# Optimization experiments

Hardware: AMD Instinct MI355X
Metric: run time of the kernel (lower is better)

Reference implementation:

```python
import jax, jax.numpy as jnp
import numpy as np

N, K, F, H, C = 16384, 16, 3, 64, 10


def setup_inputs() -> dict:
    key = jax.random.key(0)
    ks = jax.random.split(key, 6)
    pos = jax.random.normal(ks[0], (N, F), jnp.float32)
    batch = jnp.zeros((N,), jnp.int32)  # single graph
    W1 = jax.random.normal(ks[1], (2 * F, H), jnp.float32) * 0.1
    b1 = jnp.zeros((H,), jnp.float32)
    W2 = jax.random.normal(ks[2], (2 * H, H), jnp.float32) * 0.1
    b2 = jnp.zeros((H,), jnp.float32)
    Wc = jax.random.normal(ks[3], (H, C), jnp.float32) * 0.1
    bc = jnp.zeros((C,), jnp.float32)
    return {"pos": pos, "batch": batch, "W1": W1, "b1": b1,
            "W2": W2, "b2": b2, "Wc": Wc, "bc": bc}


def knn_graph(pos, k):
    # brute-force knn with self-loops (loop=True): self has distance 0
    sq = jnp.sum(pos * pos, axis=1)
    d = sq[:, None] + sq[None, :] - 2.0 * (pos @ pos.T)  # [N, N]
    _, idx = jax.lax.top_k(-d, k)  # [N, k] nearest neighbor indices (incl. self)
    return idx


def edge_conv(x, idx, W, b):
    # message for edge j->i: Linear(concat(x_i, x_j - x_i)); aggregate by max over neighbors
    n, k = idx.shape
    xi = x[:, None, :]               # [N, 1, F]
    xj = x[idx]                      # [N, k, F]
    msg = jnp.concatenate([jnp.broadcast_to(xi, (n, k, x.shape[1])), xj - xi], axis=-1)
    m = msg @ W + b                  # [N, k, H]
    return jnp.max(m, axis=1)        # [N, H]


def reference(pos, batch, W1, b1, W2, b2, Wc, bc):
    idx = knn_graph(pos, K)
    h = jax.nn.relu(edge_conv(pos, idx, W1, b1))
    h = jax.nn.relu(edge_conv(h, idx, W2, b2))
    g = jax.ops.segment_max(h, batch, num_segments=1)  # global max pool -> [1, H]
    return g @ Wc + bc
```

## Files before the change

### kernel.cpp

```cpp
#include <hip/hip_runtime.h>

#define NPTS 16384
#define KNN 16
#define HID 64
#define NCLS 10

#define WPB 4
#define QPB 8
#define SCAP 128
#define GRPQ 32
#define NITER 16
#define TPAD 576

typedef float v2f __attribute__((ext_vector_type(2)));

__device__ __forceinline__ v2f pdist(v2f Qx, v2f Qy, v2f Qz, v2f X, v2f Y, v2f Z, v2f W) {
    return __builtin_elementwise_fma(Qx, X,
            __builtin_elementwise_fma(Qy, Y,
             __builtin_elementwise_fma(Qz, Z, W)));
}

__device__ __forceinline__ float distm2(float qx, float qy, float qz, float4 c) {
    return fmaf(qx, c.x, fmaf(qy, c.y, fmaf(qz, c.z, c.w)));
}

__device__ __forceinline__ float __frfl(float x) {
    return __int_as_float(__builtin_amdgcn_readfirstlane(__float_as_int(x)));
}

__device__ __forceinline__ unsigned long long dkey(float v, int j) {
    unsigned u = __float_as_uint(v);
    u = (u & 0x80000000u) ? ~u : (u | 0x80000000u);
    return ((unsigned long long)u << 32) | (unsigned)j;
}

__device__ __forceinline__ unsigned long long shfl_xor_u64(unsigned long long x, int m) {
    unsigned hi = (unsigned)__shfl_xor((int)(x >> 32), m, 64);
    unsigned lo = (unsigned)__shfl_xor((int)(x & 0xffffffffu), m, 64);
    return ((unsigned long long)hi << 32) | lo;
}

__device__ __forceinline__ void wave_top16_16(unsigned long long (&key)[16], int lane,
                                              int q, int* __restrict__ idx) {
    int outj = 0x7fffffff;
    for (int r = 0; r < 16; ++r) {
        unsigned long long gm = key[0];
#pragma unroll
        for (int s = 1; s < 16; ++s) gm = key[s] < gm ? key[s] : gm;
#pragma unroll
        for (int st = 1; st < 64; st <<= 1) {
            unsigned long long o = shfl_xor_u64(gm, st);
            gm = o < gm ? o : gm;
        }
        if (lane == r) outj = (int)(gm & 0xffffffffu);
#pragma unroll
        for (int s = 0; s < 16; ++s)
            if (key[s] == gm) key[s] = ~0ull;
    }
    if (lane < 16) idx[q * KNN + lane] = outj;
}

__global__ void prep_kernel(const float* __restrict__ pos, float4* __restrict__ pos4,
                            float4* __restrict__ pm2, float4* __restrict__ pm2t) {
    int i = blockIdx.x * 256 + threadIdx.x;
    if (i < NPTS) {
        float x = pos[3 * i], y = pos[3 * i + 1], z = pos[3 * i + 2];
        float sq = fmaf(x, x, fmaf(y, y, z * z));
        pos4[i] = make_float4(x, y, z, sq);
        pm2[i] = make_float4(-2.f * x, -2.f * y, -2.f * z, sq);
    }
    if (i < NPTS / 2) {
        int p = i;
        float x0 = pos[6 * p],     y0 = pos[6 * p + 1], z0 = pos[6 * p + 2];
        float x1 = pos[6 * p + 3], y1 = pos[6 * p + 4], z1 = pos[6 * p + 5];
        float w0 = fmaf(x0, x0, fmaf(y0, y0, z0 * z0));
        float w1 = fmaf(x1, x1, fmaf(y1, y1, z1 * z1));
        int g = p >> 6, l = p & 63;
        pm2t[g * 128 + l]      = make_float4(-2.f * x0, -2.f * x1, -2.f * y0, -2.f * y1);
        pm2t[g * 128 + 64 + l] = make_float4(-2.f * z0, -2.f * z1, w0, w1);
    }
}

__global__ __launch_bounds__(256) void knn_kernel(const float4* __restrict__ pos4,
                                                  const float4* __restrict__ pm2,
                                                  const float4* __restrict__ pm2t,
                                                  int* __restrict__ idx) {
    __shared__ unsigned long long keys[QPB][SCAP];
    __shared__ int knt[QPB];
    __shared__ float smin[QPB][WPB][16];
    int tid = threadIdx.x;
    int lane = tid & 63;
    int w = tid >> 6;
    int qb = blockIdx.x * QPB;
    v2f Qx[QPB], Qy[QPB], Qz[QPB];
#pragma unroll
    for (int i = 0; i < QPB; ++i) {
        float4 t4 = pos4[qb + i];
        float ax = __frfl(t4.x), ay = __frfl(t4.y), az = __frfl(t4.z);
        Qx[i] = (v2f){ax, ax}; Qy[i] = (v2f){ay, ay}; Qz[i] = (v2f){az, az};
    }
    const float4* pt = pm2t + (size_t)w * (GRPQ * 128) + lane;

    float mn[QPB];
#pragma unroll
    for (int i = 0; i < QPB; ++i) mn[i] = INFINITY;
    {
        float4 aXY0 = pt[0],   aZW0 = pt[64],  aXY1 = pt[128], aZW1 = pt[192];
        float4 bXY0 = pt[256], bZW0 = pt[320], bXY1 = pt[384], bZW1 = pt[448];
        int off = 512;
#pragma unroll 2
        for (int t = 0; t < NITER; ++t) {
            v2f X0 = {aXY0.x, aXY0.y}, Y0 = {aXY0.z, aXY0.w};
            v2f Z0 = {aZW0.x, aZW0.y}, W0 = {aZW0.z, aZW0.w};
            v2f X1 = {aXY1.x, aXY1.y}, Y1 = {aXY1.z, aXY1.w};
            v2f Z1 = {aZW1.x, aZW1.y}, W1 = {aZW1.z, aZW1.w};
#pragma unroll
            for (int i = 0; i < QPB; ++i) {
                v2f D0 = pdist(Qx[i], Qy[i], Qz[i], X0, Y0, Z0, W0);
                v2f D1 = pdist(Qx[i], Qy[i], Qz[i], X1, Y1, Z1, W1);
                mn[i] = fminf(mn[i], fminf(D0.x, D0.y));
                mn[i] = fminf(mn[i], fminf(D1.x, D1.y));
            }
            aXY0 = bXY0; aZW0 = bZW0; aXY1 = bXY1; aZW1 = bZW1;
            bXY0 = pt[off]; bZW0 = pt[off + 64]; bXY1 = pt[off + 128]; bZW1 = pt[off + 192];
            off += 256;
        }
    }
#pragma unroll
    for (int i = 0; i < QPB; ++i) {
        float m = mn[i];
        m = fminf(m, __shfl_xor(m, 16, 64));
        m = fminf(m, __shfl_xor(m, 32, 64));
        if (lane < 16) smin[i][w][lane] = m;
    }
    if (tid < QPB) knt[tid] = 0;
    __syncthreads();

    float tq[QPB];
#pragma unroll
    for (int i = 0; i < QPB; ++i) {
        int s = lane & 15;
        float m = fminf(fminf(smin[i][0][s], smin[i][1][s]),
                        fminf(smin[i][2][s], smin[i][3][s]));
        m = fmaxf(m, __shfl_xor(m, 1, 64));
        m = fmaxf(m, __shfl_xor(m, 2, 64));
        m = fmaxf(m, __shfl_xor(m, 4, 64));
        m = fmaxf(m, __shfl_xor(m, 8, 64));
        tq[i] = __frfl(m);
    }

    {
        float4 aXY0 = pt[0],   aZW0 = pt[64],  aXY1 = pt[128], aZW1 = pt[192];
        float4 bXY0 = pt[256], bZW0 = pt[320], bXY1 = pt[384], bZW1 = pt[448];
        int off = 512;
        int pbase = w * (GRPQ * 64);
#pragma unroll 2
        for (int t = 0; t < NITER; ++t) {
            v2f X0 = {aXY0.x, aXY0.y}, Y0 = {aXY0.z, aXY0.w};
            v2f Z0 = {aZW0.x, aZW0.y}, W0 = {aZW0.z, aZW0.w};
            v2f X1 = {aXY1.x, aXY1.y}, Y1 = {aXY1.z, aXY1.w};
            v2f Z1 = {aZW1.x, aZW1.y}, W1 = {aZW1.z, aZW1.w};
            int j00 = 2 * (pbase + t * 128 + lane);
            int j10 = j00 + 128;
#pragma unroll
            for (int i = 0; i < QPB; ++i) {
                v2f D0 = pdist(Qx[i], Qy[i], Qz[i], X0, Y0, Z0, W0);
                v2f D1 = pdist(Qx[i], Qy[i], Qz[i], X1, Y1, Z1, W1);
                float m01 = fminf(fminf(D0.x, D0.y), fminf(D1.x, D1.y));
                if (__any(m01 <= tq[i])) {
                    if (D0.x <= tq[i]) { int s = atomicAdd(&knt[i], 1); if (s < SCAP) keys[i][s] = dkey(D0.x, j00); }
                    if (D0.y <= tq[i]) { int s = atomicAdd(&knt[i], 1); if (s < SCAP) keys[i][s] = dkey(D0.y, j00 + 1); }
                    if (D1.x <= tq[i]) { int s = atomicAdd(&knt[i], 1); if (s < SCAP) keys[i][s] = dkey(D1.x, j10); }
                    if (D1.y <= tq[i]) { int s = atomicAdd(&knt[i], 1); if (s < SCAP) keys[i][s] = dkey(D1.y, j10 + 1); }
                }
            }
            aXY0 = bXY0; aZW0 = bZW0; aXY1 = bXY1; aZW1 = bZW1;
            bXY0 = pt[off]; bZW0 = pt[off + 64]; bXY1 = pt[off + 128]; bZW1 = pt[off + 448 - 256];
            bXY1 = pt[off + 128]; bZW1 = pt[off + 192];
            off += 256;
        }
    }
    __syncthreads();

#pragma unroll
    for (int e = 0; e < 2; ++e) {
        int qi = w * 2 + e;
        int q = qb + qi;
        int ntot = knt[qi];
        if (ntot <= SCAP) {
            unsigned long long k0 = (lane < ntot) ? keys[qi][lane] : ~0ull;
            unsigned long long k1 = (lane + 64 < ntot) ? keys[qi][lane + 64] : ~0ull;
            int r0 = 0, r1 = 0;
            int t = 0;
            for (; t + 8 <= ntot; t += 8) {
                unsigned long long a0 = keys[qi][t + 0], a1 = keys[qi][t + 1];
                unsigned long long a2 = keys[qi][t + 2], a3 = keys[qi][t + 3];
                unsigned long long a4 = keys[qi][t + 4], a5 = keys[qi][t + 5];
                unsigned long long a6 = keys[qi][t + 6], a7 = keys[qi][t + 7];
                r0 += (int)(a0 < k0) + (int)(a1 < k0) + (int)(a2 < k0) + (int)(a3 < k0)
                    + (int)(a4 < k0) + (int)(a5 < k0) + (int)(a6 < k0) + (int)(a7 < k0);
                r1 += (int)(a0 < k1) + (int)(a1 < k1) + (int)(a2 < k1) + (int)(a3 < k1)
                    + (int)(a4 < k1) + (int)(a5 < k1) + (int)(a6 < k1) + (int)(a7 < k1);
            }
            for (; t < ntot; ++t) {
                unsigned long long k = keys[qi][t];
                r0 += (int)(k < k0);
                r1 += (int)(k < k1);
            }
            if (lane < ntot && r0 < KNN) idx[q * KNN + r0] = (int)(k0 & 0xffffffffu);
            if (lane + 64 < ntot && r1 < KNN) idx[q * KNN + r1] = (int)(k1 & 0xffffffffu);
        } else {
            float tqq = tq[qi];
            float ax = Qx[qi].x, ay = Qy[qi].x, az = Qz[qi].x;
            unsigned long long key[16];
#pragma unroll
            for (int u = 0; u < 16; ++u) key[u] = ~0ull;
            for (int j = lane; j < NPTS; j += 64) {
                float v = distm2(ax, ay, az, pm2[j]);
                unsigned long long k = dkey(v, j);
                if (v <= tqq && k < key[15]) {
#pragma unroll
                    for (int s = 0; s < 16; ++s) {
                        unsigned long long a = k < key[s] ? k : key[s];
                        unsigned long long b = k < key[s] ? key[s] : k;
                        key[s] = a;
                        k = b;
                    }
                }
            }
            wave_top16_16(key, lane, q, idx);
        }
    }
}

__global__ __launch_bounds__(256) void ec12_kernel(const float4* __restrict__ pos4,
                                                   const int* __restrict__ idx,
                                                   const float* __restrict__ W1,
                                                   const float* __restrict__ b1,
                                                   const float* __restrict__ W2,
                                                   const float* __restrict__ b2,
                                                   float* __restrict__ C2,
                                                   float* __restrict__ Y2) {
    __shared__ float h1s[16][64];
    int t = threadIdx.x & 63;
    int w = threadIdx.x >> 6;
    int pb = blockIdx.x * 16 + w * 4;
    float w0 = W1[0 * HID + t], w1 = W1[1 * HID + t], w2 = W1[2 * HID + t];
    float v0 = W1[3 * HID + t], v1 = W1[4 * HID + t], v2 = W1[5 * HID + t];
    float bt1 = b1[t];
#pragma unroll
    for (int i = 0; i < 4; ++i) {
        int p = pb + i;
        float4 xi = pos4[p];
        float C = bt1 + xi.x * (w0 - v0) + xi.y * (w1 - v1) + xi.z * (w2 - v2);
        const int4* ip = (const int4*)(idx + (size_t)p * KNN);
        int4 n0 = ip[0], n1 = ip[1], n2 = ip[2], n3 = ip[3];
        int jj[16] = {n0.x, n0.y, n0.z, n0.w, n1.x, n1.y, n1.z, n1.w,
                      n2.x, n2.y, n2.z, n2.w, n3.x, n3.y, n3.z, n3.w};
        float m = -INFINITY;
#pragma unroll
        for (int k = 0; k < KNN; ++k) {
            float4 xj = pos4[jj[k]];
            m = fmaxf(m, fmaf(xj.x, v0, fmaf(xj.y, v1, xj.z * v2)));
        }
        h1s[w * 4 + i][t] = fmaxf(C + m, 0.f);
    }
    __syncthreads();
    float aa[4] = {0.f, 0.f, 0.f, 0.f};
    float ab[4] = {0.f, 0.f, 0.f, 0.f};
#pragma unroll 8
    for (int f = 0; f < 64; ++f) {
        float wa = W2[f * HID + t];
        float wb = W2[(64 + f) * HID + t];
#pragma unroll
        for (int i = 0; i < 4; ++i) {
            float h = h1s[w * 4 + i][f];
            aa[i] = fmaf(h, wa, aa[i]);
            ab[i] = fmaf(h, wb, ab[i]);
        }
    }
    float bt = b2[t];
#pragma unroll
    for (int i = 0; i < 4; ++i) {
        C2[(pb + i) * HID + t] = bt + aa[i] - ab[i];
        Y2[(pb + i) * HID + t] = ab[i];
    }
}

__global__ __launch_bounds__(256) void ec2_maxpool_kernel(const float* __restrict__ C2,
                                                          const float* __restrict__ Y2,
                                                          const int* __restrict__ idx,
                                                          float* __restrict__ gpartial) {
    int t = threadIdx.x & 63;
    int lp = threadIdx.x >> 6;
    int p = blockIdx.x * 4 + lp;
    const int4* ip = (const int4*)(idx + (size_t)p * KNN);
    int4 n0 = ip[0], n1 = ip[1], n2 = ip[2], n3 = ip[3];
    int jj[16] = {n0.x, n0.y, n0.z, n0.w, n1.x, n1.y, n1.z, n1.w,
                  n2.x, n2.y, n2.z, n2.w, n3.x, n3.y, n3.z, n3.w};
    float m = -INFINITY;
#pragma unroll
    for (int k = 0; k < KNN; ++k) {
        m = fmaxf(m, Y2[jj[k] * HID + t]);
    }
    float val = fmaxf(C2[p * HID + t] + m, 0.f);
    __shared__ float red[4][64];
    red[lp][t] = val;
    __syncthreads();
    if (lp == 0) {
        float g = fmaxf(fmaxf(red[0][t], red[1][t]), fmaxf(red[2][t], red[3][t]));
        gpartial[blockIdx.x * 64 + t] = g;
    }
}

__global__ __launch_bounds__(256) void greduce2_kernel(const float* __restrict__ gpartial,
                                                       float* __restrict__ gp2) {
    __shared__ float red[4][64];
    int f = threadIdx.x & 63;
    int w = threadIdx.x >> 6;
    int r0 = blockIdx.x * 16 + w * 4;
    float m = -INFINITY;
#pragma unroll
    for (int r = 0; r < 4; ++r) m = fmaxf(m, gpartial[(r0 + r) * 64 + f]);
    red[w][f] = m;
    __syncthreads();
    if (w == 0)
        gp2[blockIdx.x * 64 + f] =
            fmaxf(fmaxf(red[0][f], red[1][f]), fmaxf(red[2][f], red[3][f]));
}

__global__ __launch_bounds__(256) void tail2_kernel(const float* __restrict__ gp2,
                                                    const float* __restrict__ Wc,
                                                    const float* __restrict__ bc,
                                                    float* __restrict__ out) {
    __shared__ float red[4][64];
    __shared__ float g[64];
    int f = threadIdx.x & 63;
    int w = threadIdx.x >> 6;
    float m = -INFINITY;
    for (int i = w; i < 256; i += 4) m = fmaxf(m, gp2[i * 64 + f]);
    red[w][f] = m;
    __syncthreads();
    if (w == 0) g[f] = fmaxf(fmaxf(red[0][f], red[1][f]), fmaxf(red[2][f], red[3][f]));
    __syncthreads();
    if (threadIdx.x < NCLS) {
        float a = bc[threadIdx.x];
#pragma unroll
        for (int h = 0; h < HID; ++h) a = fmaf(g[h], Wc[h * NCLS + threadIdx.x], a);
        out[threadIdx.x] = a;
    }
}

extern "C" void kernel_launch(void* const* d_in, const int* in_sizes, int n_in,
                              void* d_out, int out_size, void* d_ws, size_t ws_size,
                              hipStream_t stream) {
    const float* pos = (const float*)d_in[0];
    const float* W1 = (const float*)d_in[2];
    const float* b1 = (const float*)d_in[3];
    const float* W2 = (const float*)d_in[4];
    const float* b2 = (const float*)d_in[5];
    const float* Wc = (const float*)d_in[6];
    const float* bc = (const float*)d_in[7];
    float* out = (float*)d_out;

    char* ws = (char*)d_ws;
    size_t o = 0;
    auto alloc = [&](size_t bytes) { size_t r = o; o += (bytes + 255) & ~size_t(255); return r; };
    size_t fm = (size_t)NPTS * HID * 4;
    size_t o_pos4 = alloc((size_t)NPTS * 16);
    size_t o_pm2 = alloc((size_t)NPTS * 16);
    size_t o_pm2t = alloc((size_t)(NPTS + TPAD) * 16);
    size_t o_idx = alloc((size_t)NPTS * KNN * 4);
    size_t o_C2 = alloc(fm);
    size_t o_Y2 = alloc(fm);
    size_t o_gp = alloc((size_t)(NPTS / 4) * HID * 4);
    size_t o_gp2 = alloc((size_t)256 * HID * 4);

    float4* pos4 = (float4*)(ws + o_pos4);
    float4* pm2 = (float4*)(ws + o_pm2);
    float4* pm2t = (float4*)(ws + o_pm2t);
    int* idx = (int*)(ws + o_idx);
    float* C2 = (float*)(ws + o_C2);
    float* Y2 = (float*)(ws + o_Y2);
    float* gp = (float*)(ws + o_gp);
    float* gp2 = (float*)(ws + o_gp2);

    hipMemsetAsync(pm2t + NPTS, 0, TPAD * sizeof(float4), stream);

    prep_kernel<<<NPTS / 256, 256, 0, stream>>>(pos, pos4, pm2, pm2t);
    knn_kernel<<<NPTS / QPB, 256, 0, stream>>>(pos4, pm2, pm2t, idx);
    ec12_kernel<<<NPTS / 16, 256, 0, stream>>>(pos4, idx, W1, b1, W2, b2, C2, Y2);
    ec2_maxpool_kernel<<<NPTS / 4, 256, 0, stream>>>(C2, Y2, idx, gp);
    greduce2_kernel<<<256, 256, 0, stream>>>(gp, gp2);
    tail2_kernel<<<1, 256, 0, stream>>>(gp2, Wc, bc, out);
}
```

Baseline: 301.4 us.

## Split KNN into separate threshold and selection kernels with per-wave full scans

The KNN kernel is split in two. A tau kernel has each wave scan all points for 4 queries and compute the per-query distance threshold without shared-memory reduction. A selection kernel then reads the thresholds from global memory and does only the candidate-collection pass. This removes the in-block barrier between the min pass and the selection pass and changes the work split, at the cost of an extra launch and an extra global buffer. It also adds a fallback path for queries that collect fewer than KNN candidates.

```diff
diff --git a/kernel.cpp b/kernel.cpp
--- a/kernel.cpp
+++ b/kernel.cpp
@@ -10,6 +10,8 @@
 #define SCAP 128
 #define GRPQ 32
 #define NITER 16
+#define NGRP (NPTS / 128)
+#define TQW 4
 #define TPAD 576
 
 typedef float v2f __attribute__((ext_vector_type(2)));
@@ -81,86 +83,94 @@
     }
 }
 
-__global__ __launch_bounds__(256) void knn_kernel(const float4* __restrict__ pos4,
-                                                  const float4* __restrict__ pm2,
-                                                  const float4* __restrict__ pm2t,
-                                                  int* __restrict__ idx) {
+__global__ __launch_bounds__(256) void knn_tau_kernel(const float4* __restrict__ pos4,
+                                                      const float4* __restrict__ pm2t,
+                                                      float* __restrict__ tqg) {
+    int lane = threadIdx.x & 63;
+    int w = threadIdx.x >> 6;
+    int q0 = (blockIdx.x * 4 + w) * TQW;
+    v2f Qx[TQW], Qy[TQW], Qz[TQW];
+#pragma unroll
+    for (int i = 0; i < TQW; ++i) {
+        float4 t4 = pos4[q0 + i];
+        float ax = __frfl(t4.x), ay = __frfl(t4.y), az = __frfl(t4.z);
+        Qx[i] = (v2f){ax, ax}; Qy[i] = (v2f){ay, ay}; Qz[i] = (v2f){az, az};
+    }
+    const float4* pt = pm2t + lane;
+    float mn[TQW];
+#pragma unroll
+    for (int i = 0; i < TQW; ++i) mn[i] = INFINITY;
+    {
+        float4 aXY0 = pt[0],   aZW0 = pt[64],  aXY1 = pt[128], aZW1 = pt[192];
+        float4 bXY0 = pt[256], bZW0 = pt[320], bXY1 = pt[384], bZW1 = pt[448];
+        int off = 512;
+#pragma unroll 2
+        for (int t = 0; t < NGRP / 2; ++t) {
+            v2f X0 = {aXY0.x, aXY0.y}, Y0 = {aXY0.z, aXY0.w};
+            v2f Z0 = {aZW0.x, aZW0.y}, W0 = {aZW0.z, aZW0.w};
+            v2f X1 = {aXY1.x, aXY1.y}, Y1 = {aXY1.z, aXY1.w};
+            v2f Z1 = {aZW1.x, aZW1.y}, W1 = {aZW1.z, aZW1.w};
+#pragma unroll
+            for (int i = 0; i < TQW; ++i) {
+                v2f D0 = pdist(Qx[i], Qy[i], Qz[i], X0, Y0, Z0, W0);
+                v2f D1 = pdist(Qx[i], Qy[i], Qz[i], X1, Y1, Z1, W1);
+                mn[i] = fminf(mn[i], fminf(D0.x, D0.y));
+                mn[i] = fminf(mn[i], fminf(D1.x, D1.y));
+            }
+            aXY0 = bXY0; aZW0 = bZW0; aXY1 = bXY1; aZW1 = bZW1;
+            bXY0 = pt[off]; bZW0 = pt[off + 64];
+            bXY1 = pt[off + 128]; bZW1 = pt[off + 192];
+            off += 256;
+        }
+    }
+#pragma unroll
+    for (int i = 0; i < TQW; ++i) {
+        float m = mn[i];
+        m = fminf(m, __shfl_xor(m, 16, 64));
+        m = fminf(m, __shfl_xor(m, 32, 64));
+        m = fmaxf(m, __shfl_xor(m, 1, 64));
+        m = fmaxf(m, __shfl_xor(m, 2, 64));
+        m = fmaxf(m, __shfl_xor(m, 4, 64));
+        m = fmaxf(m, __shfl_xor(m, 8, 64));
+        if (lane == 0) tqg[q0 + i] = m;
+    }
+}
+
+__global__ __launch_bounds__(256) void knn_sel_kernel(const float4* __restrict__ pos4,
+                                                      const float4* __restrict__ pm2,
+                                                      const float4* __restrict__ pm2t,
+                                                      const float* __restrict__ tqg,
+                                                      int* __restrict__ idx) {
     __shared__ unsigned long long keys[QPB][SCAP];
     __shared__ int knt[QPB];
-    __shared__ float smin[QPB][WPB][16];
     int tid = threadIdx.x;
     int lane = tid & 63;
     int w = tid >> 6;
     int qb = blockIdx.x * QPB;
     v2f Qx[QPB], Qy[QPB], Qz[QPB];
+    float tq[QPB];
 #pragma unroll
     for (int i = 0; i < QPB; ++i) {
         float4 t4 = pos4[qb + i];
         float ax = __frfl(t4.x), ay = __frfl(t4.y), az = __frfl(t4.z);
         Qx[i] = (v2f){ax, ax}; Qy[i] = (v2f){ay, ay}; Qz[i] = (v2f){az, az};
-    }
+        tq[i] = __frfl(tqg[qb + i]);
+    }
+    if (tid < QPB) knt[tid] = 0;
+    __syncthreads();
+
     const float4* pt = pm2t + (size_t)w * (GRPQ * 128) + lane;
-
-    float mn[QPB];
-#pragma unroll
-    for (int i = 0; i < QPB; ++i) mn[i] = INFINITY;
     {
         float4 aXY0 = pt[0],   aZW0 = pt[64],  aXY1 = pt[128], aZW1 = pt[192];
         float4 bXY0 = pt[256], bZW0 = pt[320], bXY1 = pt[384], bZW1 = pt[448];
         int off = 512;
+        int j00 = 2 * (w * (GRPQ * 64) + lane);
 #pragma unroll 2
         for (int t = 0; t < NITER; ++t) {
             v2f X0 = {aXY0.x, aXY0.y}, Y0 = {aXY0.z, aXY0.w};
             v2f Z0 = {aZW0.x, aZW0.y}, W0 = {aZW0.z, aZW0.w};
             v2f X1 = {aXY1.x, aXY1.y}, Y1 = {aXY1.z, aXY1.w};
             v2f Z1 = {aZW1.x, aZW1.y}, W1 = {aZW1.z, aZW1.w};
-#pragma unroll
-            for (int i = 0; i < QPB; ++i) {
-                v2f D0 = pdist(Qx[i], Qy[i], Qz[i], X0, Y0, Z0, W0);
-                v2f D1 = pdist(Qx[i], Qy[i], Qz[i], X1, Y1, Z1, W1);
-                mn[i] = fminf(mn[i], fminf(D0.x, D0.y));
-                mn[i] = fminf(mn[i], fminf(D1.x, D1.y));
-            }
-            aXY0 = bXY0; aZW0 = bZW0; aXY1 = bXY1; aZW1 = bZW1;
-            bXY0 = pt[off]; bZW0 = pt[off + 64]; bXY1 = pt[off + 128]; bZW1 = pt[off + 192];
-            off += 256;
-        }
-    }
-#pragma unroll
-    for (int i = 0; i < QPB; ++i) {
-        float m = mn[i];
-        m = fminf(m, __shfl_xor(m, 16, 64));
-        m = fminf(m, __shfl_xor(m, 32, 64));
-        if (lane < 16) smin[i][w][lane] = m;
-    }
-    if (tid < QPB) knt[tid] = 0;
-    __syncthreads();
-
-    float tq[QPB];
-#pragma unroll
-    for (int i = 0; i < QPB; ++i) {
-        int s = lane & 15;
-        float m = fminf(fminf(smin[i][0][s], smin[i][1][s]),
-                        fminf(smin[i][2][s], smin[i][3][s]));
-        m = fmaxf(m, __shfl_xor(m, 1, 64));
-        m = fmaxf(m, __shfl_xor(m, 2, 64));
-        m = fmaxf(m, __shfl_xor(m, 4, 64));
-        m = fmaxf(m, __shfl_xor(m, 8, 64));
-        tq[i] = __frfl(m);
-    }
-
-    {
-        float4 aXY0 = pt[0],   aZW0 = pt[64],  aXY1 = pt[128], aZW1 = pt[192];
-        float4 bXY0 = pt[256], bZW0 = pt[320], bXY1 = pt[384], bZW1 = pt[448];
-        int off = 512;
-        int pbase = w * (GRPQ * 64);
-#pragma unroll 2
-        for (int t = 0; t < NITER; ++t) {
-            v2f X0 = {aXY0.x, aXY0.y}, Y0 = {aXY0.z, aXY0.w};
-            v2f Z0 = {aZW0.x, aZW0.y}, W0 = {aZW0.z, aZW0.w};
-            v2f X1 = {aXY1.x, aXY1.y}, Y1 = {aXY1.z, aXY1.w};
-            v2f Z1 = {aZW1.x, aZW1.y}, W1 = {aZW1.z, aZW1.w};
-            int j00 = 2 * (pbase + t * 128 + lane);
             int j10 = j00 + 128;
 #pragma unroll
             for (int i = 0; i < QPB; ++i) {
@@ -175,9 +185,10 @@
                 }
             }
             aXY0 = bXY0; aZW0 = bZW0; aXY1 = bXY1; aZW1 = bZW1;
-            bXY0 = pt[off]; bZW0 = pt[off + 64]; bXY1 = pt[off + 128]; bZW1 = pt[off + 448 - 256];
+            bXY0 = pt[off]; bZW0 = pt[off + 64];
             bXY1 = pt[off + 128]; bZW1 = pt[off + 192];
             off += 256;
+            j00 += 256;
         }
     }
     __syncthreads();
@@ -187,7 +198,7 @@
         int qi = w * 2 + e;
         int q = qb + qi;
         int ntot = knt[qi];
-        if (ntot <= SCAP) {
+        if (ntot >= KNN && ntot <= SCAP) {
             unsigned long long k0 = (lane < ntot) ? keys[qi][lane] : ~0ull;
             unsigned long long k1 = (lane + 64 < ntot) ? keys[qi][lane + 64] : ~0ull;
             int r0 = 0, r1 = 0;
@@ -210,7 +221,7 @@
             if (lane < ntot && r0 < KNN) idx[q * KNN + r0] = (int)(k0 & 0xffffffffu);
             if (lane + 64 < ntot && r1 < KNN) idx[q * KNN + r1] = (int)(k1 & 0xffffffffu);
         } else {
-            float tqq = tq[qi];
+            float tqq = (ntot > SCAP) ? tq[qi] : INFINITY;
             float ax = Qx[qi].x, ay = Qy[qi].x, az = Qz[qi].x;
             unsigned long long key[16];
 #pragma unroll
@@ -370,6 +381,7 @@
     size_t o_pos4 = alloc((size_t)NPTS * 16);
     size_t o_pm2 = alloc((size_t)NPTS * 16);
     size_t o_pm2t = alloc((size_t)(NPTS + TPAD) * 16);
+    size_t o_tqg = alloc((size_t)NPTS * 4);
     size_t o_idx = alloc((size_t)NPTS * KNN * 4);
     size_t o_C2 = alloc(fm);
     size_t o_Y2 = alloc(fm);
@@ -379,6 +391,7 @@
     float4* pos4 = (float4*)(ws + o_pos4);
     float4* pm2 = (float4*)(ws + o_pm2);
     float4* pm2t = (float4*)(ws + o_pm2t);
+    float* tqg = (float*)(ws + o_tqg);
     int* idx = (int*)(ws + o_idx);
     float* C2 = (float*)(ws + o_C2);
     float* Y2 = (float*)(ws + o_Y2);
@@ -388,7 +401,8 @@
     hipMemsetAsync(pm2t + NPTS, 0, TPAD * sizeof(float4), stream);
 
     prep_kernel<<<NPTS / 256, 256, 0, stream>>>(pos, pos4, pm2, pm2t);
-    knn_kernel<<<NPTS / QPB, 256, 0, stream>>>(pos4, pm2, pm2t, idx);
+    knn_tau_kernel<<<NPTS / (4 * TQW), 256, 0, stream>>>(pos4, pm2t, tqg);
+    knn_sel_kernel<<<NPTS / QPB, 256, 0, stream>>>(pos4, pm2, pm2t, tqg, idx);
     ec12_kernel<<<NPTS / 16, 256, 0, stream>>>(pos4, idx, W1, b1, W2, b2, C2, Y2);
     ec2_maxpool_kernel<<<NPTS / 4, 256, 0, stream>>>(C2, Y2, idx, gp);
     greduce2_kernel<<<256, 256, 0, stream>>>(gp, gp2);
```

Result: no change. 306.3 us (+1.6%).
